# Kernel optimization log

Measured on AMD Instinct MI355X. Metric: run time of the kernel, lower is better.

Reference implementation:

```python
import jax, jax.numpy as jnp
import numpy as np

N_NODES = 50000
N_EDGES = 1000000


def _edge_conv(x, src, dst, W, b, n_nodes):
    """PyG EdgeConv: msg = nn(cat([x_i, x_j - x_i])), aggr=max over incoming edges."""
    xi = x[dst]                      # [E, C] target features
    xj = x[src]                      # [E, C] source features
    m = jnp.concatenate([xi, xj - xi], axis=-1)          # [E, 2C]
    m = jax.nn.relu(m @ W + b)                           # [E, C_out]
    out = jax.ops.segment_max(m, dst, num_segments=n_nodes)  # [N, C_out]
    # empty segments produce -inf; PyG fills with 0
    return jnp.where(jnp.isfinite(out), out, 0.0)


def setup_inputs() -> dict:
    key = jax.random.key(0)
    ks = jax.random.split(key, 12)
    x = jax.random.normal(ks[0], (N_NODES, 3), dtype=jnp.float32)
    edge_index = jax.random.randint(ks[1], (2, N_EDGES), 0, N_NODES, dtype=jnp.int64)

    def lin(k, fan_in, fan_out):
        s = 1.0 / np.sqrt(fan_in)
        kw, kb = jax.random.split(k)
        W = jax.random.uniform(kw, (fan_in, fan_out), jnp.float32, -s, s)
        b = jax.random.uniform(kb, (fan_out,), jnp.float32, -s, s)
        return W, b

    W1, b1 = lin(ks[2], 6, 64)       # conv1 MLP([3*2, 64])
    W2, b2 = lin(ks[3], 128, 128)    # conv2 MLP([64*2, 128])
    W3, b3 = lin(ks[4], 256, 512)    # conv3 MLP([128*2, 512])
    W4, b4 = lin(ks[5], 512, 256)    # lin1 MLP([512, 256])
    W5, b5 = lin(ks[6], 256, 3)      # lin1 final Linear(256, 3)
    return {"x": x, "edge_index": edge_index,
            "W1": W1, "b1": b1, "W2": W2, "b2": b2, "W3": W3, "b3": b3,
            "W4": W4, "b4": b4, "W5": W5, "b5": b5}


def reference(x, edge_index, W1, b1, W2, b2, W3, b3, W4, b4, W5, b5):
    src = edge_index[0]  # x_j
    dst = edge_index[1]  # x_i (aggregation target)
    n = x.shape[0]
    x1 = _edge_conv(x, src, dst, W1, b1, n)    # [N, 64]
    x2 = _edge_conv(x1, src, dst, W2, b2, n)   # [N, 128]
    x3 = _edge_conv(x2, src, dst, W3, b3, n)   # [N, 512]
    x4 = jax.nn.relu(x3 @ W4 + b4) @ W5 + b5   # [N, 3]
    return x + x4
```

## Files before the change

kernel.cpp:

```cpp
#include <hip/hip_runtime.h>

static constexpr int NN = 50000;
static constexpr int NE = 1000000;

typedef short bf16x8 __attribute__((ext_vector_type(8)));
typedef float f32x4 __attribute__((ext_vector_type(4)));
typedef unsigned short u16x2 __attribute__((ext_vector_type(2)));

__device__ inline float bf2f_raw(unsigned short u) {
    return __uint_as_float(((unsigned int)u) << 16);
}
__device__ inline unsigned short f2bf(float f) {
    unsigned int u = __float_as_uint(f);
    u += 0x7fffu + ((u >> 16) & 1u);
    return (unsigned short)(u >> 16);
}
__device__ inline unsigned short f2bfs(float f) {
    unsigned short b = f2bf(f);
    return (b & 0x8000u) ? (unsigned short)(~b) : (unsigned short)(b | 0x8000u);
}
__device__ inline float unsrt2f(unsigned short v) {
    unsigned short b = (v & 0x8000u) ? (unsigned short)(v ^ 0x8000u)
                                     : (unsigned short)(~v);
    return bf2f_raw(b);
}
__device__ inline unsigned int pkmax(unsigned int a, unsigned int b) {
    u16x2 r = __builtin_elementwise_max(__builtin_bit_cast(u16x2, a),
                                        __builtin_bit_cast(u16x2, b));
    return __builtin_bit_cast(unsigned int, r);
}
__device__ inline unsigned int pack2(float f0, float f1) {
    return (unsigned int)f2bf(f0) | ((unsigned int)f2bf(f1) << 16);
}
__device__ inline unsigned int addrelu2t(unsigned int a, unsigned int t) {
    float t0 = unsrt2f((unsigned short)(t & 0xffffu));
    float t1 = unsrt2f((unsigned short)(t >> 16));
    float f0 = fmaxf(bf2f_raw((unsigned short)(a & 0xffffu)) + t0, 0.f);
    float f1 = fmaxf(bf2f_raw((unsigned short)(a >> 16)) + t1, 0.f);
    return pack2(f0, f1);
}


__global__ void setup_kernel(const float* __restrict__ x, const float* __restrict__ W1,
                             const float* __restrict__ b1, const float* __restrict__ b5,
                             const float* __restrict__ W2, const float* __restrict__ W3,
                             const float* __restrict__ W4,
                             unsigned short* __restrict__ as1, float* __restrict__ out,
                             int* __restrict__ deg, int* __restrict__ cursor,
                             unsigned short* __restrict__ Bt2,
                             unsigned short* __restrict__ Bt3,
                             unsigned short* __restrict__ W4t) {
    int t = blockIdx.x * blockDim.x + threadIdx.x;
    if (t < NN * 128) {
        int i = t >> 7, c = t & 127;
        float x0 = x[i * 3 + 0], x1 = x[i * 3 + 1], x2 = x[i * 3 + 2];
        if (c < 64) {
            float v = x0 * (W1[c] - W1[192 + c]) + x1 * (W1[64 + c] - W1[256 + c]) +
                      x2 * (W1[128 + c] - W1[320 + c]) + b1[c];
            as1[t] = f2bf(v);
        } else {
            int cs = c - 64;
            float v = x0 * W1[192 + cs] + x1 * W1[256 + cs] + x2 * W1[320 + cs];
            as1[t] = f2bfs(v);
        }
        return;
    }
    t -= NN * 128;
    if (t < NN * 3) { out[t] = x[t] + b5[t % 3]; return; }
    t -= NN * 3;
    if (t < NN) { deg[t] = 0; return; }
    t -= NN;
    if (t < NN) { cursor[t] = 0; return; }
    t -= NN;
    if (t < 8192) {
        int k = t / 128, c = t % 128;
        float wt = W2[k * 128 + c];
        float wb = W2[(64 + k) * 128 + c];
        Bt2[c * 64 + k] = f2bf(wt - wb);
        Bt2[(128 + c) * 64 + k] = f2bf(wb);
        return;
    }
    t -= 8192;
    if (t < 65536) {
        int k = t / 512, c = t % 512;
        float wt = W3[k * 512 + c];
        float wb = W3[(128 + k) * 512 + c];
        Bt3[c * 128 + k] = f2bf(wt - wb);
        Bt3[(512 + c) * 128 + k] = f2bf(wb);
        return;
    }
    t -= 65536;
    if (t < 131072) {
        int k = t / 256, n = t % 256;
        W4t[n * 512 + k] = f2bf(W4[k * 256 + n]);
    }
}


__global__ void hist_kernel(const int* __restrict__ dst, int* __restrict__ deg) {
    int e = blockIdx.x * blockDim.x + threadIdx.x;
    if (e < NE) atomicAdd(&deg[dst[e]], 1);
}

__global__ __launch_bounds__(1024) void scan_kernel(const int* __restrict__ deg,
                                                    int* __restrict__ rowstart) {
    __shared__ int wave_sums[16];
    constexpr int CH = (NN + 1023) / 1024;
    int tid = threadIdx.x;
    int lane = tid & 63;
    int wave = tid >> 6;
    int base = tid * CH;
    int vals[CH];
    int sum = 0;
    #pragma unroll
    for (int i = 0; i < CH; ++i) {
        int idx = base + i;
        vals[i] = (idx < NN) ? deg[idx] : 0;
        sum += vals[i];
    }
    int x = sum;
    #pragma unroll
    for (int off = 1; off < 64; off <<= 1) {
        int y = __shfl_up(x, off);
        if (lane >= off) x += y;
    }
    if (lane == 63) wave_sums[wave] = x;
    __syncthreads();
    if (wave == 0 && lane < 16) {
        int s = wave_sums[lane];
        #pragma unroll
        for (int off = 1; off < 16; off <<= 1) {
            int y = __shfl_up(s, off);
            if (lane >= off) s += y;
        }
        wave_sums[lane] = s;
    }
    __syncthreads();
    int run = (wave ? wave_sums[wave - 1] : 0) + x - sum;
    #pragma unroll
    for (int i = 0; i < CH; ++i) {
        int idx = base + i;
        if (idx < NN) rowstart[idx] = run;
        run += vals[i];
    }
    if (tid == 1023) rowstart[NN] = run;
}

__global__ void scatter_kernel(const int* __restrict__ src, const int* __restrict__ dst,
                               const int* __restrict__ rowstart, int* __restrict__ cursor,
                               int* __restrict__ csr) {
    int e = blockIdx.x * blockDim.x + threadIdx.x;
    if (e < NE) {
        int d = dst[e];
        int pos = atomicAdd(&cursor[d], 1);
        csr[rowstart[d] + pos] = src[e];
    }
}


__global__ __launch_bounds__(256) void edge_fused_conv1_kernel(
    const unsigned short* __restrict__ as, const int* __restrict__ rowstart,
    const int* __restrict__ csr, unsigned short* __restrict__ x1) {
    int wid = (blockIdx.x * 256 + threadIdx.x) >> 6;
    int lane = threadIdx.x & 63;
    if (wid >= NN) return;
    int e0 = __builtin_amdgcn_readfirstlane(rowstart[wid]);
    int e1 = __builtin_amdgcn_readfirstlane(rowstart[wid + 1]);
    int h = lane >> 5, c0 = (lane & 31) * 2;
    unsigned int t = 0u;
    const unsigned short* sb = as + 64 + c0;
    int nedge = e1 - e0;
    for (int base = 0; base < nedge; base += 64) {
        int rem = nedge - base;
        int myj = csr[(lane < rem) ? (e0 + base + lane) : e0];
        int cnt = rem < 64 ? rem : 64;
        int cp = (cnt + 7) & ~7;
        unsigned int v[4];
        #pragma unroll
        for (int k = 0; k < 4; ++k) {
            int j = __shfl(myj, 2 * k + h);
            v[k] = *(const unsigned int*)(sb + (size_t)j * 128);
        }
        for (int q = 8; q < cp; q += 8) {
            unsigned int w[4];
            #pragma unroll
            for (int k = 0; k < 4; ++k) {
                int j = __shfl(myj, q + 2 * k + h);
                w[k] = *(const unsigned int*)(sb + (size_t)j * 128);
            }
            #pragma unroll
            for (int k = 0; k < 4; ++k) t = pkmax(t, v[k]);
            #pragma unroll
            for (int k = 0; k < 4; ++k) v[k] = w[k];
        }
        #pragma unroll
        for (int k = 0; k < 4; ++k) t = pkmax(t, v[k]);
    }
    t = pkmax(t, __shfl_xor(t, 32));
    if (h == 0) {
        unsigned int av = *(const unsigned int*)(as + (size_t)wid * 128 + c0);
        *(unsigned int*)(x1 + (size_t)wid * 64 + c0) = addrelu2t(av, t);
    }
}


__global__ __launch_bounds__(256) void edge_fused128_kernel(
    const unsigned short* __restrict__ as, const int* __restrict__ rowstart,
    const int* __restrict__ csr, unsigned short* __restrict__ xout) {
    int wid = (blockIdx.x * 256 + threadIdx.x) >> 6;
    int lane = threadIdx.x & 63;
    if (wid >= NN) return;
    int e0 = __builtin_amdgcn_readfirstlane(rowstart[wid]);
    int e1 = __builtin_amdgcn_readfirstlane(rowstart[wid + 1]);
    unsigned int t = 0u;
    const unsigned short* sb = as + 128 + (size_t)lane * 2;
    int nedge = e1 - e0;
    for (int base = 0; base < nedge; base += 64) {
        int rem = nedge - base;
        int myj = csr[(lane < rem) ? (e0 + base + lane) : e0];
        int cnt = rem < 64 ? rem : 64;
        int cp = (cnt + 7) & ~7;
        unsigned int v[8];
        #pragma unroll
        for (int k = 0; k < 8; ++k) {
            int j = __shfl(myj, k);
            v[k] = *(const unsigned int*)(sb + (size_t)j * 256);
        }
        for (int q = 8; q < cp; q += 8) {
            unsigned int w[8];
            #pragma unroll
            for (int k = 0; k < 8; ++k) {
                int j = __shfl(myj, q + k);
                w[k] = *(const unsigned int*)(sb + (size_t)j * 256);
            }
            #pragma unroll
            for (int k = 0; k < 8; ++k) t = pkmax(t, v[k]);
            #pragma unroll
            for (int k = 0; k < 8; ++k) v[k] = w[k];
        }
        #pragma unroll
        for (int k = 0; k < 8; ++k) t = pkmax(t, v[k]);
    }
    unsigned int av = *(const unsigned int*)(as + (size_t)wid * 256 + lane * 2);
    *(unsigned int*)(xout + (size_t)wid * 128 + lane * 2) = addrelu2t(av, t);
}


__global__ __launch_bounds__(256) void ef512_w5_kernel(
    const unsigned short* __restrict__ as, const int* __restrict__ rowstart,
    const int* __restrict__ csr, const unsigned short* __restrict__ W4t,
    const float* __restrict__ b4, const float* __restrict__ W5,
    float* __restrict__ out) {
    __shared__ __align__(16) unsigned short X[16][520];
    int wave = threadIdx.x >> 6, lane = threadIdx.x & 63;
    int tilebase = blockIdx.x * 16;

    const unsigned short* sb = as + 512 + (size_t)lane * 8;
    for (int i = 0; i < 4; ++i) {
        int node = tilebase + wave * 4 + i;
        int e0 = __builtin_amdgcn_readfirstlane(rowstart[node]);
        int e1 = __builtin_amdgcn_readfirstlane(rowstart[node + 1]);
        unsigned int m0 = 0u, m1 = 0u, m2 = 0u, m3 = 0u;
        int nedge = e1 - e0;
        for (int base = 0; base < nedge; base += 64) {
            int rem = nedge - base;
            int myj = csr[(lane < rem) ? (e0 + base + lane) : e0];
            int cnt = rem < 64 ? rem : 64;
            int cp = (cnt + 3) & ~3;
            int j0 = __shfl(myj, 0), j1 = __shfl(myj, 1);
            int j2 = __shfl(myj, 2), j3 = __shfl(myj, 3);
            uint4 v0 = *(const uint4*)(sb + (size_t)j0 * 1024);
            uint4 v1 = *(const uint4*)(sb + (size_t)j1 * 1024);
            uint4 v2 = *(const uint4*)(sb + (size_t)j2 * 1024);
            uint4 v3 = *(const uint4*)(sb + (size_t)j3 * 1024);
            for (int q = 4; q < cp; q += 4) {
                int k0 = __shfl(myj, q + 0), k1 = __shfl(myj, q + 1);
                int k2 = __shfl(myj, q + 2), k3 = __shfl(myj, q + 3);
                uint4 w0 = *(const uint4*)(sb + (size_t)k0 * 1024);
                uint4 w1 = *(const uint4*)(sb + (size_t)k1 * 1024);
                uint4 w2 = *(const uint4*)(sb + (size_t)k2 * 1024);
                uint4 w3 = *(const uint4*)(sb + (size_t)k3 * 1024);
                m0 = pkmax(m0, v0.x); m1 = pkmax(m1, v0.y);
                m2 = pkmax(m2, v0.z); m3 = pkmax(m3, v0.w);
                m0 = pkmax(m0, v1.x); m1 = pkmax(m1, v1.y);
                m2 = pkmax(m2, v1.z); m3 = pkmax(m3, v1.w);
                m0 = pkmax(m0, v2.x); m1 = pkmax(m1, v2.y);
                m2 = pkmax(m2, v2.z); m3 = pkmax(m3, v2.w);
                m0 = pkmax(m0, v3.x); m1 = pkmax(m1, v3.y);
                m2 = pkmax(m2, v3.z); m3 = pkmax(m3, v3.w);
                v0 = w0; v1 = w1; v2 = w2; v3 = w3;
            }
            m0 = pkmax(m0, v0.x); m1 = pkmax(m1, v0.y);
            m2 = pkmax(m2, v0.z); m3 = pkmax(m3, v0.w);
            m0 = pkmax(m0, v1.x); m1 = pkmax(m1, v1.y);
            m2 = pkmax(m2, v1.z); m3 = pkmax(m3, v1.w);
            m0 = pkmax(m0, v2.x); m1 = pkmax(m1, v2.y);
            m2 = pkmax(m2, v2.z); m3 = pkmax(m3, v2.w);
            m0 = pkmax(m0, v3.x); m1 = pkmax(m1, v3.y);
            m2 = pkmax(m2, v3.z); m3 = pkmax(m3, v3.w);
        }
        uint4 av = *(const uint4*)(as + (size_t)node * 1024 + lane * 8);
        uint4 o;
        o.x = addrelu2t(av.x, m0);
        o.y = addrelu2t(av.y, m1);
        o.z = addrelu2t(av.z, m2);
        o.w = addrelu2t(av.w, m3);
        *(uint4*)&X[wave * 4 + i][lane * 8] = o;
    }
    __syncthreads();

    int quad = lane >> 4, l16 = lane & 15;
    int colbase = wave * 64;
    f32x4 acc4[4] = {};
    for (int kc = 0; kc < 16; ++kc) {
        bf16x8 afr = *(const bf16x8*)&X[l16][kc * 32 + quad * 8];
        #pragma unroll
        for (int nt = 0; nt < 4; ++nt) {
            int col = colbase + nt * 16 + l16;
            bf16x8 bfr = *(const bf16x8*)&W4t[(size_t)col * 512 + kc * 32 + quad * 8];
            acc4[nt] = __builtin_amdgcn_mfma_f32_16x16x32_bf16(afr, bfr, acc4[nt], 0, 0, 0);
        }
    }
    float b4v[4], w5r[4][3];
    #pragma unroll
    for (int nt = 0; nt < 4; ++nt) {
        int col = colbase + nt * 16 + l16;
        b4v[nt] = b4[col];
        w5r[nt][0] = W5[col * 3 + 0];
        w5r[nt][1] = W5[col * 3 + 1];
        w5r[nt][2] = W5[col * 3 + 2];
    }
    #pragma unroll
    for (int r = 0; r < 4; ++r) {
        int row = tilebase + quad * 4 + r;
        float p0 = 0.f, p1 = 0.f, p2 = 0.f;
        #pragma unroll
        for (int nt = 0; nt < 4; ++nt) {
            float h = fmaxf(acc4[nt][r] + b4v[nt], 0.f);
            p0 += h * w5r[nt][0];
            p1 += h * w5r[nt][1];
            p2 += h * w5r[nt][2];
        }
        #pragma unroll
        for (int m = 8; m; m >>= 1) {
            p0 += __shfl_xor(p0, m);
            p1 += __shfl_xor(p1, m);
            p2 += __shfl_xor(p2, m);
        }
        if (l16 == 0) {
            atomicAdd(&out[row * 3 + 0], p0);
            atomicAdd(&out[row * 3 + 1], p1);
            atomicAdd(&out[row * 3 + 2], p2);
        }
    }
}


template<int K, int NT>
__global__ __launch_bounds__(256) void mfma_gemm_nloop_kernel(
    const unsigned short* __restrict__ A, const unsigned short* __restrict__ Bt,
    const float* __restrict__ bias, int bias_n,
    unsigned short* __restrict__ C, int M) {
    constexpr int KC = K / 32;
    constexpr int N = NT * 128;
    __shared__ __align__(16) unsigned short Asl[KC][128 * 40];
    __shared__ __align__(16) unsigned short Bsl[128 * 40];
    int tid = threadIdx.x;
    int mbase = blockIdx.x * 128;
    int wave = tid >> 6, lane = tid & 63;
    int wm = (wave >> 1) * 64, wn = (wave & 1) * 64;
    int quad = lane >> 4, l16 = lane & 15;

    #pragma unroll
    for (int c = tid; c < KC * 512; c += 256) {
        int kc = c >> 9, rem = c & 511;
        int r = rem >> 2, kk = (rem & 3) * 8;
        uint4 va = make_uint4(0u, 0u, 0u, 0u);
        int gr = mbase + r;
        if (gr < M) va = *(const uint4*)&A[(size_t)gr * K + kc * 32 + kk];
        *(uint4*)&Asl[kc][r * 40 + kk] = va;
    }

    for (int nt = 0; nt < NT; ++nt) {
        int nbase = nt * 128;
        f32x4 acc[4][4] = {};
        for (int kc = 0; kc < KC; ++kc) {
            __syncthreads();
            #pragma unroll
            for (int h = 0; h < 2; ++h) {
                int c = tid + h * 256;
                int r = c >> 2, kk = (c & 3) * 8;
                uint4 vb = *(const uint4*)&Bt[(size_t)(nbase + r) * K + kc * 32 + kk];
                *(uint4*)&Bsl[r * 40 + kk] = vb;
            }
            __syncthreads();
            bf16x8 af[4], bfr[4];
            #pragma unroll
            for (int tt = 0; tt < 4; ++tt) {
                af[tt]  = *(const bf16x8*)&Asl[kc][(wm + tt * 16 + l16) * 40 + quad * 8];
                bfr[tt] = *(const bf16x8*)&Bsl[(wn + tt * 16 + l16) * 40 + quad * 8];
            }
            #pragma unroll
            for (int mt = 0; mt < 4; ++mt)
                #pragma unroll
                for (int ntt = 0; ntt < 4; ++ntt)
                    acc[mt][ntt] = __builtin_amdgcn_mfma_f32_16x16x32_bf16(
                        af[mt], bfr[ntt], acc[mt][ntt], 0, 0, 0);
        }
        #pragma unroll
        for (int mt = 0; mt < 4; ++mt) {
            #pragma unroll
            for (int r = 0; r < 4; ++r) {
                int row = mbase + wm + mt * 16 + quad * 4 + r;
                if (row >= M) continue;
                #pragma unroll
                for (int ntt = 0; ntt < 4; ++ntt) {
                    int col = nbase + wn + ntt * 16 + l16;
                    float v = acc[mt][ntt][r];
                    unsigned short o;
                    if (col < bias_n) o = f2bf(v + bias[col]);
                    else o = f2bfs(v);
                    C[(size_t)row * N + col] = o;
                }
            }
        }
    }
}

__global__ void fallback_copy_kernel(const float* __restrict__ x, float* __restrict__ out) {
    int t = blockIdx.x * blockDim.x + threadIdx.x;
    if (t < NN * 3) out[t] = x[t];
}


extern "C" void kernel_launch(void* const* d_in, const int* in_sizes, int n_in,
                              void* d_out, int out_size, void* d_ws, size_t ws_size,
                              hipStream_t stream) {
    const float* x  = (const float*)d_in[0];
    const int*   ei = (const int*)d_in[1];
    const float* W1 = (const float*)d_in[2];
    const float* b1 = (const float*)d_in[3];
    const float* W2 = (const float*)d_in[4];
    const float* b2 = (const float*)d_in[5];
    const float* W3 = (const float*)d_in[6];
    const float* b3 = (const float*)d_in[7];
    const float* W4 = (const float*)d_in[8];
    const float* b4 = (const float*)d_in[9];
    const float* W5 = (const float*)d_in[10];
    const float* b5 = (const float*)d_in[11];
    float* out = (float*)d_out;

    char* p = (char*)d_ws;
    auto alloc = [&](size_t bytes) -> void* {
        void* r = (void*)p;
        p += (bytes + 255) & ~(size_t)255;
        return r;
    };
    int* deg      = (int*)alloc((size_t)NN * 4);
    int* rowstart = (int*)alloc((size_t)(NN + 1) * 4);
    int* cursor   = (int*)alloc((size_t)NN * 4);
    int* csr      = (int*)alloc((size_t)NE * 4);
    unsigned short* Bt2 = (unsigned short*)alloc(256 * 64 * 2);
    unsigned short* Bt3 = (unsigned short*)alloc(1024 * 128 * 2);
    unsigned short* W4t = (unsigned short*)alloc(256 * 512 * 2);
    unsigned short* x1 = (unsigned short*)alloc((size_t)NN * 64 * 2);
    unsigned short* x2 = (unsigned short*)alloc((size_t)NN * 128 * 2);
    unsigned short* as_slab = (unsigned short*)alloc((size_t)NN * 1024 * 2);
    size_t need = (size_t)(p - (char*)d_ws);
    if (ws_size < need) {
        fallback_copy_kernel<<<(NN * 3 + 255) / 256, 256, 0, stream>>>(x, out);
        return;
    }

    const int* src = ei;
    const int* dst = ei + NE;

    constexpr int SETUP_T = NN * 128 + NN * 3 + NN + NN + 8192 + 65536 + 131072;
    setup_kernel<<<(SETUP_T + 255) / 256, 256, 0, stream>>>(
        x, W1, b1, b5, W2, W3, W4, as_slab, out, deg, cursor, Bt2, Bt3, W4t);

    hist_kernel<<<(NE + 255) / 256, 256, 0, stream>>>(dst, deg);
    scan_kernel<<<1, 1024, 0, stream>>>(deg, rowstart);
    scatter_kernel<<<(NE + 255) / 256, 256, 0, stream>>>(src, dst, rowstart, cursor, csr);

    edge_fused_conv1_kernel<<<12500, 256, 0, stream>>>(as_slab, rowstart, csr, x1);

    mfma_gemm_nloop_kernel<64, 2><<<391, 256, 0, stream>>>(
        x1, Bt2, b2, 128, as_slab, NN);
    edge_fused128_kernel<<<12500, 256, 0, stream>>>(as_slab, rowstart, csr, x2);

    mfma_gemm_nloop_kernel<128, 8><<<391, 256, 0, stream>>>(
        x2, Bt3, b3, 512, as_slab, NN);

    ef512_w5_kernel<<<NN / 16, 256, 0, stream>>>(
        as_slab, rowstart, csr, W4t, b4, W5, out);
}
```

Measured before the change: 597.9 us.

## Use scalar-broadcast CSR indices with deeper unrolled gathers in edge max kernels

The three edge-aggregation kernels change how they read neighbor indices. Each lane no longer loads a slice of CSR and shuffles it out; the wave now reads indices uniformly via readfirstlane, clamping the tail to the last edge. Each iteration issues 16 gathers (8 for the 512-wide kernel), and the max goes into two accumulators to shorten the dependency chain. Conv1 now uses all 64 lanes on one 16-bit channel each instead of splitting edges across half-waves, which narrows its per-lane loads. The clamped tail re-reads duplicate rows, which is harmless for max but adds redundant loads on low-degree nodes.

```diff
diff --git a/kernel.cpp b/kernel.cpp
--- a/kernel.cpp
+++ b/kernel.cpp
@@ -28,6 +28,11 @@
     u16x2 r = __builtin_elementwise_max(__builtin_bit_cast(u16x2, a),
                                         __builtin_bit_cast(u16x2, b));
     return __builtin_bit_cast(unsigned int, r);
+}
+__device__ inline uint4 pkmax4(uint4 a, uint4 b) {
+    a.x = pkmax(a.x, b.x); a.y = pkmax(a.y, b.y);
+    a.z = pkmax(a.z, b.z); a.w = pkmax(a.w, b.w);
+    return a;
 }
 __device__ inline unsigned int pack2(float f0, float f1) {
     return (unsigned int)f2bf(f0) | ((unsigned int)f2bf(f1) << 16);
@@ -166,41 +171,33 @@
     if (wid >= NN) return;
     int e0 = __builtin_amdgcn_readfirstlane(rowstart[wid]);
     int e1 = __builtin_amdgcn_readfirstlane(rowstart[wid + 1]);
-    int h = lane >> 5, c0 = (lane & 31) * 2;
-    unsigned int t = 0u;
-    const unsigned short* sb = as + 64 + c0;
     int nedge = e1 - e0;
-    for (int base = 0; base < nedge; base += 64) {
-        int rem = nedge - base;
-        int myj = csr[(lane < rem) ? (e0 + base + lane) : e0];
-        int cnt = rem < 64 ? rem : 64;
-        int cp = (cnt + 7) & ~7;
-        unsigned int v[4];
-        #pragma unroll
-        for (int k = 0; k < 4; ++k) {
-            int j = __shfl(myj, 2 * k + h);
-            v[k] = *(const unsigned int*)(sb + (size_t)j * 128);
-        }
-        for (int q = 8; q < cp; q += 8) {
-            unsigned int w[4];
-            #pragma unroll
-            for (int k = 0; k < 4; ++k) {
-                int j = __shfl(myj, q + 2 * k + h);
-                w[k] = *(const unsigned int*)(sb + (size_t)j * 128);
-            }
-            #pragma unroll
-            for (int k = 0; k < 4; ++k) t = pkmax(t, v[k]);
-            #pragma unroll
-            for (int k = 0; k < 4; ++k) v[k] = w[k];
-        }
-        #pragma unroll
-        for (int k = 0; k < 4; ++k) t = pkmax(t, v[k]);
-    }
-    t = pkmax(t, __shfl_xor(t, 32));
-    if (h == 0) {
-        unsigned int av = *(const unsigned int*)(as + (size_t)wid * 128 + c0);
-        *(unsigned int*)(x1 + (size_t)wid * 64 + c0) = addrelu2t(av, t);
-    }
+    unsigned int mA = 0u, mB = 0u;
+    if (nedge > 0) {
+        int last = nedge - 1;
+        for (int e = 0; e < nedge; e += 16) {
+            int jj[16];
+            #pragma unroll
+            for (int k = 0; k < 16; ++k) {
+                int idx = e + k; if (idx > last) idx = last;
+                jj[k] = __builtin_amdgcn_readfirstlane(csr[e0 + idx]);
+            }
+            unsigned int v[16];
+            #pragma unroll
+            for (int k = 0; k < 16; ++k)
+                v[k] = *(const unsigned short*)(as + (size_t)jj[k] * 128 + 64 + lane);
+            #pragma unroll
+            for (int k = 0; k < 16; ++k) {
+                if (k & 1) mB = mB > v[k] ? mB : v[k];
+                else       mA = mA > v[k] ? mA : v[k];
+            }
+        }
+    }
+    unsigned int m = mA > mB ? mA : mB;
+    unsigned short a = as[(size_t)wid * 128 + lane];
+    float t = unsrt2f((unsigned short)m);
+    float f = fmaxf(bf2f_raw(a) + t, 0.f);
+    x1[(size_t)wid * 64 + lane] = f2bf(f);
 }
 
 
@@ -212,35 +209,29 @@
     if (wid >= NN) return;
     int e0 = __builtin_amdgcn_readfirstlane(rowstart[wid]);
     int e1 = __builtin_amdgcn_readfirstlane(rowstart[wid + 1]);
-    unsigned int t = 0u;
-    const unsigned short* sb = as + 128 + (size_t)lane * 2;
     int nedge = e1 - e0;
-    for (int base = 0; base < nedge; base += 64) {
-        int rem = nedge - base;
-        int myj = csr[(lane < rem) ? (e0 + base + lane) : e0];
-        int cnt = rem < 64 ? rem : 64;
-        int cp = (cnt + 7) & ~7;
-        unsigned int v[8];
-        #pragma unroll
-        for (int k = 0; k < 8; ++k) {
-            int j = __shfl(myj, k);
-            v[k] = *(const unsigned int*)(sb + (size_t)j * 256);
-        }
-        for (int q = 8; q < cp; q += 8) {
-            unsigned int w[8];
-            #pragma unroll
-            for (int k = 0; k < 8; ++k) {
-                int j = __shfl(myj, q + k);
-                w[k] = *(const unsigned int*)(sb + (size_t)j * 256);
-            }
-            #pragma unroll
-            for (int k = 0; k < 8; ++k) t = pkmax(t, v[k]);
-            #pragma unroll
-            for (int k = 0; k < 8; ++k) v[k] = w[k];
-        }
-        #pragma unroll
-        for (int k = 0; k < 8; ++k) t = pkmax(t, v[k]);
-    }
+    unsigned int mA = 0u, mB = 0u;
+    if (nedge > 0) {
+        int last = nedge - 1;
+        for (int e = 0; e < nedge; e += 16) {
+            int jj[16];
+            #pragma unroll
+            for (int k = 0; k < 16; ++k) {
+                int idx = e + k; if (idx > last) idx = last;
+                jj[k] = __builtin_amdgcn_readfirstlane(csr[e0 + idx]);
+            }
+            unsigned int v[16];
+            #pragma unroll
+            for (int k = 0; k < 16; ++k)
+                v[k] = *(const unsigned int*)(as + (size_t)jj[k] * 256 + 128 + lane * 2);
+            #pragma unroll
+            for (int k = 0; k < 16; ++k) {
+                if (k & 1) mB = pkmax(mB, v[k]);
+                else       mA = pkmax(mA, v[k]);
+            }
+        }
+    }
+    unsigned int t = pkmax(mA, mB);
     unsigned int av = *(const unsigned int*)(as + (size_t)wid * 256 + lane * 2);
     *(unsigned int*)(xout + (size_t)wid * 128 + lane * 2) = addrelu2t(av, t);
 }
@@ -255,56 +246,39 @@
     int wave = threadIdx.x >> 6, lane = threadIdx.x & 63;
     int tilebase = blockIdx.x * 16;
 
-    const unsigned short* sb = as + 512 + (size_t)lane * 8;
     for (int i = 0; i < 4; ++i) {
         int node = tilebase + wave * 4 + i;
         int e0 = __builtin_amdgcn_readfirstlane(rowstart[node]);
         int e1 = __builtin_amdgcn_readfirstlane(rowstart[node + 1]);
-        unsigned int m0 = 0u, m1 = 0u, m2 = 0u, m3 = 0u;
         int nedge = e1 - e0;
-        for (int base = 0; base < nedge; base += 64) {
-            int rem = nedge - base;
-            int myj = csr[(lane < rem) ? (e0 + base + lane) : e0];
-            int cnt = rem < 64 ? rem : 64;
-            int cp = (cnt + 3) & ~3;
-            int j0 = __shfl(myj, 0), j1 = __shfl(myj, 1);
-            int j2 = __shfl(myj, 2), j3 = __shfl(myj, 3);
-            uint4 v0 = *(const uint4*)(sb + (size_t)j0 * 1024);
-            uint4 v1 = *(const uint4*)(sb + (size_t)j1 * 1024);
-            uint4 v2 = *(const uint4*)(sb + (size_t)j2 * 1024);
-            uint4 v3 = *(const uint4*)(sb + (size_t)j3 * 1024);
-            for (int q = 4; q < cp; q += 4) {
-                int k0 = __shfl(myj, q + 0), k1 = __shfl(myj, q + 1);
-                int k2 = __shfl(myj, q + 2), k3 = __shfl(myj, q + 3);
-                uint4 w0 = *(const uint4*)(sb + (size_t)k0 * 1024);
-                uint4 w1 = *(const uint4*)(sb + (size_t)k1 * 1024);
-                uint4 w2 = *(const uint4*)(sb + (size_t)k2 * 1024);
-                uint4 w3 = *(const uint4*)(sb + (size_t)k3 * 1024);
-                m0 = pkmax(m0, v0.x); m1 = pkmax(m1, v0.y);
-                m2 = pkmax(m2, v0.z); m3 = pkmax(m3, v0.w);
-                m0 = pkmax(m0, v1.x); m1 = pkmax(m1, v1.y);
-                m2 = pkmax(m2, v1.z); m3 = pkmax(m3, v1.w);
-                m0 = pkmax(m0, v2.x); m1 = pkmax(m1, v2.y);
-                m2 = pkmax(m2, v2.z); m3 = pkmax(m3, v2.w);
-                m0 = pkmax(m0, v3.x); m1 = pkmax(m1, v3.y);
-                m2 = pkmax(m2, v3.z); m3 = pkmax(m3, v3.w);
-                v0 = w0; v1 = w1; v2 = w2; v3 = w3;
-            }
-            m0 = pkmax(m0, v0.x); m1 = pkmax(m1, v0.y);
-            m2 = pkmax(m2, v0.z); m3 = pkmax(m3, v0.w);
-            m0 = pkmax(m0, v1.x); m1 = pkmax(m1, v1.y);
-            m2 = pkmax(m2, v1.z); m3 = pkmax(m3, v1.w);
-            m0 = pkmax(m0, v2.x); m1 = pkmax(m1, v2.y);
-            m2 = pkmax(m2, v2.z); m3 = pkmax(m3, v2.w);
-            m0 = pkmax(m0, v3.x); m1 = pkmax(m1, v3.y);
-            m2 = pkmax(m2, v3.z); m3 = pkmax(m3, v3.w);
-        }
+        uint4 mA = make_uint4(0u, 0u, 0u, 0u), mB = make_uint4(0u, 0u, 0u, 0u);
+        if (nedge > 0) {
+            int last = nedge - 1;
+            for (int e = 0; e < nedge; e += 8) {
+                int jj[8];
+                #pragma unroll
+                for (int k = 0; k < 8; ++k) {
+                    int idx = e + k; if (idx > last) idx = last;
+                    jj[k] = __builtin_amdgcn_readfirstlane(csr[e0 + idx]);
+                }
+                uint4 v[8];
+                #pragma unroll
+                for (int k = 0; k < 8; ++k)
+                    v[k] = *(const uint4*)(as + (size_t)jj[k] * 1024 + 512 + lane * 8);
+                #pragma unroll
+                for (int k = 0; k < 8; ++k) {
+                    if (k & 1) mB = pkmax4(mB, v[k]);
+                    else       mA = pkmax4(mA, v[k]);
+                }
+            }
+        }
+        uint4 m = pkmax4(mA, mB);
         uint4 av = *(const uint4*)(as + (size_t)node * 1024 + lane * 8);
         uint4 o;
-        o.x = addrelu2t(av.x, m0);
-        o.y = addrelu2t(av.y, m1);
-        o.z = addrelu2t(av.z, m2);
-        o.w = addrelu2t(av.w, m3);
+        o.x = addrelu2t(av.x, m.x);
+        o.y = addrelu2t(av.y, m.y);
+        o.z = addrelu2t(av.z, m.z);
+        o.w = addrelu2t(av.w, m.w);
         *(uint4*)&X[wave * 4 + i][lane * 8] = o;
     }
     __syncthreads();
```

Result: no change. 599.7 us (+0.3%).
